# Kernel tuning notes

Hardware: AMD Instinct MI355X
Metric: run time of the kernel (lower is better)

Reference implementation:

```python
import jax, jax.numpy as jnp
import numpy as np

N, K, D = 32768, 8192, 256


def setup_inputs() -> dict:
    key = jax.random.key(0)
    k1, k2 = jax.random.split(key)
    x = jax.random.normal(k1, (N, D), dtype=jnp.float32)
    vectors = jax.random.normal(k2, (K, D), dtype=jnp.float32)  # codebook
    return {"x": x, "vectors": vectors}


def reference(x, vectors):
    # torch.cdist(x[:,None,:], vectors[None]) followed by argmin over K.
    # Euclidean distance is monotone in squared distance, so argmin over the
    # without a sqrt, matching the original math exactly for the returned ids.
    x2 = jnp.sum(x * x, axis=-1, keepdims=True)          # [N, 1]
    c2 = jnp.sum(vectors * vectors, axis=-1)             # [K]
    d2 = x2 + c2 - 2.0 * jnp.matmul(x, vectors.T)        # [N, K]
    indices = jnp.argmin(d2, axis=-1)                    # [N]
    return indices.astype(jnp.int32)
```

## Files before the change

kernel.cpp:

```cpp
#include <hip/hip_runtime.h>
#include <stdint.h>
#include <stddef.h>


#define N_PTS 32768
#define K_CB  8192
#define D_DIM 256
#define TM 128
#define TN 128
#define SPLITK 4
#define KCHUNK (K_CB / SPLITK)
#define NTILES (KCHUNK / TN)

#define WS_XH   0
#define WS_XL   (WS_XH + N_PTS * D_DIM * 2)
#define WS_CH   (WS_XL + N_PTS * D_DIM * 2)
#define WS_CL   (WS_CH + K_CB * D_DIM * 2)
#define WS_C2   (WS_CL + K_CB * D_DIM * 2)
#define WS_PD   (WS_C2 + K_CB * 4)
#define WS_PI   (WS_PD + SPLITK * N_PTS * 4)
#define WS_END  (WS_PI + SPLITK * N_PTS * 4)

typedef _Float16 half4v __attribute__((ext_vector_type(4)));
typedef _Float16 half8v __attribute__((ext_vector_type(8)));
typedef float    f32x4  __attribute__((ext_vector_type(4)));

__device__ __forceinline__ void gld16(const void* g, void* l) {
    __builtin_amdgcn_global_load_lds(
        (const __attribute__((address_space(1))) void*)g,
        (__attribute__((address_space(3))) void*)l, 16, 0, 0);
}


__global__ void __launch_bounds__(256)
split_kernel(const float* __restrict__ src, _Float16* __restrict__ h_out,
             _Float16* __restrict__ l_out) {
    const int i = blockIdx.x * 256 + threadIdx.x;
    const float4 v = ((const float4*)src)[i];
    half4v h = {(_Float16)v.x, (_Float16)v.y, (_Float16)v.z, (_Float16)v.w};
    half4v l = {(_Float16)((v.x - (float)h[0]) * 2048.0f),
                (_Float16)((v.y - (float)h[1]) * 2048.0f),
                (_Float16)((v.z - (float)h[2]) * 2048.0f),
                (_Float16)((v.w - (float)h[3]) * 2048.0f)};
    *(half4v*)(h_out + (size_t)i * 4) = h;
    *(half4v*)(l_out + (size_t)i * 4) = l;
}

__global__ void __launch_bounds__(256)
cnorms_kernel(const float* __restrict__ vecs, float* __restrict__ c2) {
    int gwave = (blockIdx.x * 256 + threadIdx.x) >> 6;
    int lane  = threadIdx.x & 63;
    const float* src = vecs + (size_t)gwave * D_DIM;
    float4 v = ((const float4*)src)[lane];
    float s = v.x * v.x + v.y * v.y + v.z * v.z + v.w * v.w;
#pragma unroll
    for (int off = 32; off > 0; off >>= 1) s += __shfl_down(s, off, 64);
    if (lane == 0) c2[gwave] = s;
}


__global__ void __launch_bounds__(256, 2)
vq_main_fast(const _Float16* __restrict__ xh_g, const _Float16* __restrict__ xl_g,
             const _Float16* __restrict__ ch_g, const _Float16* __restrict__ cl_g,
             const float* __restrict__ c2, float* __restrict__ pd, int* __restrict__ pi) {
    __shared__ __align__(16) char lds[65536];

    const int t    = threadIdx.x;
    const int lane = t & 63;
    const int wv   = t >> 6;
    const int wy   = wv >> 1, wx = wv & 1;
    const int fr   = lane & 15;
    const int g    = lane >> 4;

    const int split = blockIdx.x & (SPLITK - 1);
    const int pbase = (blockIdx.x >> 2) * TM;
    const int kbase = split * KCHUNK;

    const int rowoff = (lane >> 3) * (D_DIM * 2) + (((lane & 7) ^ (lane >> 3)) << 4);
    const char* xh_w = (const char*)xh_g + (size_t)(pbase + wv * 32) * (D_DIM * 2) + rowoff;
    const char* xl_w = (const char*)xl_g + (size_t)(pbase + wv * 32) * (D_DIM * 2) + rowoff;
    char* ldsA_h = lds +         (wv * 32) * 128;
    char* ldsA_l = lds + 16384 + (wv * 32) * 128;
    char* ldsB_h = lds + 32768 + (wv * 32) * 128;
    char* ldsB_l = lds + 49152 + (wv * 32) * 128;

    int aoff[4][2], boff[4][2];
#pragma unroll
    for (int i = 0; i < 4; ++i)
#pragma unroll
        for (int ks = 0; ks < 2; ++ks) {
            aoff[i][ks] = (wy * 64 + i * 16 + fr) * 128 + (((ks * 4 + g) ^ (fr & 7)) << 4);
            boff[i][ks] = 32768 + (wx * 64 + i * 16 + fr) * 128 + (((ks * 4 + g) ^ (fr & 7)) << 4);
        }

    float best[16];
    int   bidx[16];
#pragma unroll
    for (int i = 0; i < 16; ++i) { best[i] = 3.4e38f; bidx[i] = 0; }

    for (int kt = 0; kt < NTILES; ++kt) {
        const int ktbase = kbase + kt * TN;
        const char* ch_w = (const char*)ch_g + (size_t)(ktbase + wv * 32) * (D_DIM * 2) + rowoff;
        const char* cl_w = (const char*)cl_g + (size_t)(ktbase + wv * 32) * (D_DIM * 2) + rowoff;

        f32x4 acc[4][4];
#pragma unroll
        for (int i = 0; i < 4; ++i)
#pragma unroll
            for (int j = 0; j < 4; ++j) {
                f32x4 z = {0.f, 0.f, 0.f, 0.f};
                acc[i][j] = z;
            }

#pragma unroll 1
        for (int dkc = 0; dkc < 4; ++dkc) {
            const int gofs = dkc * 128;
            __syncthreads();
#pragma unroll
            for (int q = 0; q < 4; ++q) {
                gld16(xh_w + q * 4096 + gofs, ldsA_h + q * 1024);
                gld16(xl_w + q * 4096 + gofs, ldsA_l + q * 1024);
                gld16(ch_w + q * 4096 + gofs, ldsB_h + q * 1024);
                gld16(cl_w + q * 4096 + gofs, ldsB_l + q * 1024);
            }
            __syncthreads();
#pragma unroll
            for (int ks = 0; ks < 2; ++ks) {
                half8v a1[4], a2[4], a3[4];
#pragma unroll
                for (int i = 0; i < 4; ++i) {
                    const char* p = lds + aoff[i][ks];
                    a1[i] = *(const half8v*)p;
                    a3[i] = *(const half8v*)(p + 16384);
                    a2[i] = a1[i] * (_Float16)4.8828125e-4f;
                }
#pragma unroll
                for (int j = 0; j < 4; ++j) {
                    const char* p = lds + boff[j][ks];
                    half8v b1 = *(const half8v*)p;
                    half8v b2 = *(const half8v*)(p + 16384);
                    half8v b3 = b1 * (_Float16)4.8828125e-4f;
#pragma unroll
                    for (int i = 0; i < 4; ++i) {
                        acc[i][j] = __builtin_amdgcn_mfma_f32_16x16x32_f16(a1[i], b1, acc[i][j], 0, 0, 0);
                        acc[i][j] = __builtin_amdgcn_mfma_f32_16x16x32_f16(a2[i], b2, acc[i][j], 0, 0, 0);
                        acc[i][j] = __builtin_amdgcn_mfma_f32_16x16x32_f16(a3[i], b3, acc[i][j], 0, 0, 0);
                    }
                }
            }
        }

#pragma unroll
        for (int j = 0; j < 4; ++j) {
            const int cg = ktbase + wx * 64 + j * 16 + fr;
            const float c2v = c2[cg];
#pragma unroll
            for (int i = 0; i < 4; ++i)
#pragma unroll
                for (int r = 0; r < 4; ++r) {
                    const float v = fmaf(-2.0f, acc[i][j][r], c2v);
                    const int s = i * 4 + r;
                    if (v < best[s]) { best[s] = v; bidx[s] = cg; }
                }
        }
    }

    __syncthreads();
    float* rd = (float*)lds;
    int*   ri = (int*)lds + 256;
#pragma unroll
    for (int i = 0; i < 4; ++i)
#pragma unroll
        for (int r = 0; r < 4; ++r) {
            float bv = best[i * 4 + r];
            int   bi = bidx[i * 4 + r];
#pragma unroll
            for (int off = 1; off < 16; off <<= 1) {
                const float ov = __shfl_xor(bv, off, 64);
                const int   oi = __shfl_xor(bi, off, 64);
                if (ov < bv || (ov == bv && oi < bi)) { bv = ov; bi = oi; }
            }
            if (fr == 0) {
                const int rowl = wy * 64 + i * 16 + g * 4 + r;
                rd[rowl * 2 + wx] = bv;
                ri[rowl * 2 + wx] = bi;
            }
        }
    __syncthreads();
    if (t < TM) {
        float b0 = rd[t * 2];
        int   i0 = ri[t * 2];
        const float b1 = rd[t * 2 + 1];
        const int   i1 = ri[t * 2 + 1];
        if (b1 < b0 || (b1 == b0 && i1 < i0)) { b0 = b1; i0 = i1; }
        pd[split * N_PTS + pbase + t] = b0;
        pi[split * N_PTS + pbase + t] = i0;
    }
}


#define BK 32
#define LS (BK + 4)

__device__ inline half8v load8(const _Float16* p) {
    half4v a = *(const half4v*)p;
    half4v b = *(const half4v*)(p + 4);
    return __builtin_shufflevector(a, b, 0, 1, 2, 3, 4, 5, 6, 7);
}

struct Trip { _Float16 h, s2, l2; };

__device__ inline Trip cvt3(float v) {
    Trip t;
    _Float16 hh = (_Float16)v;
    float hf = (float)hh;
    t.h  = hh;
    t.s2 = (_Float16)(hf * 4.8828125e-4f);
    t.l2 = (_Float16)((v - hf) * 2048.0f);
    return t;
}

__global__ void __launch_bounds__(256, 2)
vq_main_v3(const float* __restrict__ x, const float* __restrict__ vecs,
           const float* __restrict__ c2, float* __restrict__ pd, int* __restrict__ pi) {
    __shared__ _Float16 lds[6 * TM * LS];
    _Float16* xh  = lds;
    _Float16* xs2 = lds + 1 * TM * LS;
    _Float16* xl2 = lds + 2 * TM * LS;
    _Float16* ch  = lds + 3 * TM * LS;
    _Float16* cl2 = lds + 4 * TM * LS;
    _Float16* cs2 = lds + 5 * TM * LS;

    const int t     = threadIdx.x;
    const int split = blockIdx.x & (SPLITK - 1);
    const int pbase = (blockIdx.x >> 2) * TM;
    const int kbase = split * KCHUNK;

    const int lane = t & 63;
    const int wv   = t >> 6;
    const int wy   = wv >> 1, wx = wv & 1;
    const int fr   = lane & 15;
    const int g    = lane >> 4;
    const int kb   = g * 8;

    const int srow = t >> 3;
    const int sc4  = (t & 7) * 4;

    float best[16];
    int   bidx[16];
#pragma unroll
    for (int i = 0; i < 16; ++i) { best[i] = 3.4e38f; bidx[i] = 0; }

    for (int kt = 0; kt < NTILES; ++kt) {
        const int ktbase = kbase + kt * TN;
        f32x4 acc[4][4];
#pragma unroll
        for (int i = 0; i < 4; ++i)
#pragma unroll
            for (int j = 0; j < 4; ++j) {
                f32x4 z = {0.f, 0.f, 0.f, 0.f};
                acc[i][j] = z;
            }
        for (int dk = 0; dk < D_DIM; dk += BK) {
            __syncthreads();
#pragma unroll
            for (int p = 0; p < 4; ++p) {
                const int row = srow + p * 32;
                const float4 v = *(const float4*)&x[(size_t)(pbase + row) * D_DIM + dk + sc4];
                const Trip t0 = cvt3(v.x), t1 = cvt3(v.y), t2 = cvt3(v.z), t3 = cvt3(v.w);
                half4v h  = {t0.h,  t1.h,  t2.h,  t3.h};
                half4v s2 = {t0.s2, t1.s2, t2.s2, t3.s2};
                half4v l2 = {t0.l2, t1.l2, t2.l2, t3.l2};
                *(half4v*)&xh [row * LS + sc4] = h;
                *(half4v*)&xs2[row * LS + sc4] = s2;
                *(half4v*)&xl2[row * LS + sc4] = l2;
                const float4 w = *(const float4*)&vecs[(size_t)(ktbase + row) * D_DIM + dk + sc4];
                const Trip u0 = cvt3(w.x), u1 = cvt3(w.y), u2 = cvt3(w.z), u3 = cvt3(w.w);
                half4v hc = {u0.h,  u1.h,  u2.h,  u3.h};
                half4v sc = {u0.s2, u1.s2, u2.s2, u3.s2};
                half4v lc = {u0.l2, u1.l2, u2.l2, u3.l2};
                *(half4v*)&ch [row * LS + sc4] = hc;
                *(half4v*)&cs2[row * LS + sc4] = sc;
                *(half4v*)&cl2[row * LS + sc4] = lc;
            }
            __syncthreads();
            half8v a1[4], a2[4], a3[4], b1[4], b2[4], b3[4];
#pragma unroll
            for (int i = 0; i < 4; ++i) {
                const int aoff = (wy * 64 + i * 16 + fr) * LS + kb;
                a1[i] = load8(&xh [aoff]);
                a2[i] = load8(&xs2[aoff]);
                a3[i] = load8(&xl2[aoff]);
                const int boff2 = (wx * 64 + i * 16 + fr) * LS + kb;
                b1[i] = load8(&ch [boff2]);
                b2[i] = load8(&cl2[boff2]);
                b3[i] = load8(&cs2[boff2]);
            }
#pragma unroll
            for (int i = 0; i < 4; ++i)
#pragma unroll
                for (int j = 0; j < 4; ++j) {
                    acc[i][j] = __builtin_amdgcn_mfma_f32_16x16x32_f16(a1[i], b1[j], acc[i][j], 0, 0, 0);
                    acc[i][j] = __builtin_amdgcn_mfma_f32_16x16x32_f16(a2[i], b2[j], acc[i][j], 0, 0, 0);
                    acc[i][j] = __builtin_amdgcn_mfma_f32_16x16x32_f16(a3[i], b3[j], acc[i][j], 0, 0, 0);
                }
        }
#pragma unroll
        for (int j = 0; j < 4; ++j) {
            const int cg = ktbase + wx * 64 + j * 16 + fr;
            const float c2v = c2[cg];
#pragma unroll
            for (int i = 0; i < 4; ++i)
#pragma unroll
                for (int r = 0; r < 4; ++r) {
                    const float v = fmaf(-2.0f, acc[i][j][r], c2v);
                    const int s = i * 4 + r;
                    if (v < best[s]) { best[s] = v; bidx[s] = cg; }
                }
        }
    }
    __syncthreads();
    float* rd = (float*)lds;
    int*   ri = (int*)lds + 256;
#pragma unroll
    for (int i = 0; i < 4; ++i)
#pragma unroll
        for (int r = 0; r < 4; ++r) {
            float bv = best[i * 4 + r];
            int   bi = bidx[i * 4 + r];
#pragma unroll
            for (int off = 1; off < 16; off <<= 1) {
                const float ov = __shfl_xor(bv, off, 64);
                const int   oi = __shfl_xor(bi, off, 64);
                if (ov < bv || (ov == bv && oi < bi)) { bv = ov; bi = oi; }
            }
            if (fr == 0) {
                const int rowl = wy * 64 + i * 16 + g * 4 + r;
                rd[rowl * 2 + wx] = bv;
                ri[rowl * 2 + wx] = bi;
            }
        }
    __syncthreads();
    if (t < TM) {
        float b0 = rd[t * 2];
        int   i0 = ri[t * 2];
        const float b1 = rd[t * 2 + 1];
        const int   i1 = ri[t * 2 + 1];
        if (b1 < b0 || (b1 == b0 && i1 < i0)) { b0 = b1; i0 = i1; }
        pd[split * N_PTS + pbase + t] = b0;
        pi[split * N_PTS + pbase + t] = i0;
    }
}


__global__ void __launch_bounds__(256)
vq_combine(const float* __restrict__ pd, const int* __restrict__ pi,
           int* __restrict__ out) {
    const int p = blockIdx.x * 256 + threadIdx.x;
    float bb = pd[p];
    int   bi = pi[p];
#pragma unroll
    for (int s = 1; s < SPLITK; ++s) {
        const float v  = pd[s * N_PTS + p];
        const int   vi = pi[s * N_PTS + p];
        if (v < bb || (v == bb && vi < bi)) { bb = v; bi = vi; }
    }
    out[p] = bi;
}

extern "C" void kernel_launch(void* const* d_in, const int* in_sizes, int n_in,
                              void* d_out, int out_size, void* d_ws, size_t ws_size,
                              hipStream_t stream) {
    const float* x    = (const float*)d_in[0];
    const float* vecs = (const float*)d_in[1];
    int* out = (int*)d_out;
    char* ws = (char*)d_ws;

    if (ws_size >= (size_t)WS_END) {
        _Float16* xh = (_Float16*)(ws + WS_XH);
        _Float16* xl = (_Float16*)(ws + WS_XL);
        _Float16* ch = (_Float16*)(ws + WS_CH);
        _Float16* cl = (_Float16*)(ws + WS_CL);
        float* c2 = (float*)(ws + WS_C2);
        float* pd = (float*)(ws + WS_PD);
        int*   pi = (int*)(ws + WS_PI);

        hipLaunchKernelGGL(split_kernel, dim3(N_PTS * D_DIM / 4 / 256), dim3(256), 0, stream,
                           x, xh, xl);
        hipLaunchKernelGGL(split_kernel, dim3(K_CB * D_DIM / 4 / 256), dim3(256), 0, stream,
                           vecs, ch, cl);
        hipLaunchKernelGGL(cnorms_kernel, dim3(K_CB / 4), dim3(256), 0, stream,
                           vecs, c2);
        hipLaunchKernelGGL(vq_main_fast, dim3((N_PTS / TM) * SPLITK), dim3(256), 0, stream,
                           xh, xl, ch, cl, c2, pd, pi);
        hipLaunchKernelGGL(vq_combine, dim3(N_PTS / 256), dim3(256), 0, stream,
                           pd, pi, out);
    } else {
        float* c2 = (float*)ws;
        float* pd = (float*)ws + K_CB;
        int*   pi = (int*)((float*)ws + K_CB + SPLITK * N_PTS);
        hipLaunchKernelGGL(cnorms_kernel, dim3(K_CB / 4), dim3(256), 0, stream,
                           vecs, c2);
        hipLaunchKernelGGL(vq_main_v3, dim3((N_PTS / TM) * SPLITK), dim3(256), 0, stream,
                           x, vecs, c2, pd, pi);
        hipLaunchKernelGGL(vq_combine, dim3(N_PTS / 256), dim3(256), 0, stream,
                           pd, pi, out);
    }
}
```

Measured before the change: 464.4 us.

## Halve LDS tile depth for higher occupancy and fuse codebook split with norms

```diff
diff --git a/kernel.cpp b/kernel.cpp
--- a/kernel.cpp
+++ b/kernel.cpp
@@ -47,23 +47,30 @@
 }
 
 __global__ void __launch_bounds__(256)
-cnorms_kernel(const float* __restrict__ vecs, float* __restrict__ c2) {
-    int gwave = (blockIdx.x * 256 + threadIdx.x) >> 6;
-    int lane  = threadIdx.x & 63;
-    const float* src = vecs + (size_t)gwave * D_DIM;
-    float4 v = ((const float4*)src)[lane];
+csplit_norm(const float* __restrict__ vecs, _Float16* __restrict__ h_out,
+            _Float16* __restrict__ l_out, float* __restrict__ c2) {
+    const int row  = (blockIdx.x * 256 + threadIdx.x) >> 6;
+    const int lane = threadIdx.x & 63;
+    const float4 v = ((const float4*)(vecs + (size_t)row * D_DIM))[lane];
+    half4v h = {(_Float16)v.x, (_Float16)v.y, (_Float16)v.z, (_Float16)v.w};
+    half4v l = {(_Float16)((v.x - (float)h[0]) * 2048.0f),
+                (_Float16)((v.y - (float)h[1]) * 2048.0f),
+                (_Float16)((v.z - (float)h[2]) * 2048.0f),
+                (_Float16)((v.w - (float)h[3]) * 2048.0f)};
+    *(half4v*)(h_out + (size_t)row * D_DIM + lane * 4) = h;
+    *(half4v*)(l_out + (size_t)row * D_DIM + lane * 4) = l;
     float s = v.x * v.x + v.y * v.y + v.z * v.z + v.w * v.w;
 #pragma unroll
     for (int off = 32; off > 0; off >>= 1) s += __shfl_down(s, off, 64);
-    if (lane == 0) c2[gwave] = s;
-}
-
-
-__global__ void __launch_bounds__(256, 2)
+    if (lane == 0) c2[row] = s;
+}
+
+
+__global__ void __launch_bounds__(256, 4)
 vq_main_fast(const _Float16* __restrict__ xh_g, const _Float16* __restrict__ xl_g,
              const _Float16* __restrict__ ch_g, const _Float16* __restrict__ cl_g,
              const float* __restrict__ c2, float* __restrict__ pd, int* __restrict__ pi) {
-    __shared__ __align__(16) char lds[65536];
+    __shared__ __align__(16) char lds[32768];
 
     const int t    = threadIdx.x;
     const int lane = t & 63;
@@ -76,22 +83,20 @@
     const int pbase = (blockIdx.x >> 2) * TM;
     const int kbase = split * KCHUNK;
 
-    const int rowoff = (lane >> 3) * (D_DIM * 2) + (((lane & 7) ^ (lane >> 3)) << 4);
+    const int rowoff = (lane >> 2) * (D_DIM * 2) + (((lane & 3) ^ ((lane >> 2) & 3)) << 4);
     const char* xh_w = (const char*)xh_g + (size_t)(pbase + wv * 32) * (D_DIM * 2) + rowoff;
     const char* xl_w = (const char*)xl_g + (size_t)(pbase + wv * 32) * (D_DIM * 2) + rowoff;
-    char* ldsA_h = lds +         (wv * 32) * 128;
-    char* ldsA_l = lds + 16384 + (wv * 32) * 128;
-    char* ldsB_h = lds + 32768 + (wv * 32) * 128;
-    char* ldsB_l = lds + 49152 + (wv * 32) * 128;
-
-    int aoff[4][2], boff[4][2];
-#pragma unroll
-    for (int i = 0; i < 4; ++i)
-#pragma unroll
-        for (int ks = 0; ks < 2; ++ks) {
-            aoff[i][ks] = (wy * 64 + i * 16 + fr) * 128 + (((ks * 4 + g) ^ (fr & 7)) << 4);
-            boff[i][ks] = 32768 + (wx * 64 + i * 16 + fr) * 128 + (((ks * 4 + g) ^ (fr & 7)) << 4);
-        }
+    char* ldsA_h = lds +         wv * 2048;
+    char* ldsA_l = lds +  8192 + wv * 2048;
+    char* ldsB_h = lds + 16384 + wv * 2048;
+    char* ldsB_l = lds + 24576 + wv * 2048;
+
+    int aoff[4], boff[4];
+#pragma unroll
+    for (int i = 0; i < 4; ++i) {
+        aoff[i] = (wy * 64 + i * 16 + fr) * 64 + ((g ^ (fr & 3)) << 4);
+        boff[i] = 16384 + (wx * 64 + i * 16 + fr) * 64 + ((g ^ (fr & 3)) << 4);
+    }
 
     float best[16];
     int   bidx[16];
@@ -113,39 +118,36 @@
             }
 
 #pragma unroll 1
-        for (int dkc = 0; dkc < 4; ++dkc) {
-            const int gofs = dkc * 128;
+        for (int dkc = 0; dkc < 8; ++dkc) {
+            const int gofs = dkc * 64;
             __syncthreads();
 #pragma unroll
-            for (int q = 0; q < 4; ++q) {
-                gld16(xh_w + q * 4096 + gofs, ldsA_h + q * 1024);
-                gld16(xl_w + q * 4096 + gofs, ldsA_l + q * 1024);
-                gld16(ch_w + q * 4096 + gofs, ldsB_h + q * 1024);
-                gld16(cl_w + q * 4096 + gofs, ldsB_l + q * 1024);
+            for (int q = 0; q < 2; ++q) {
+                gld16(xh_w + q * 8192 + gofs, ldsA_h + q * 1024);
+                gld16(xl_w + q * 8192 + gofs, ldsA_l + q * 1024);
+                gld16(ch_w + q * 8192 + gofs, ldsB_h + q * 1024);
+                gld16(cl_w + q * 8192 + gofs, ldsB_l + q * 1024);
             }
             __syncthreads();
-#pragma unroll
-            for (int ks = 0; ks < 2; ++ks) {
-                half8v a1[4], a2[4], a3[4];
+            half8v a1[4], a2[4], a3[4];
+#pragma unroll
+            for (int i = 0; i < 4; ++i) {
+                const char* p = lds + aoff[i];
+                a1[i] = *(const half8v*)p;
+                a3[i] = *(const half8v*)(p + 8192);
+                a2[i] = a1[i] * (_Float16)4.8828125e-4f;
+            }
+#pragma unroll
+            for (int j = 0; j < 4; ++j) {
+                const char* p = lds + boff[j];
+                half8v b1 = *(const half8v*)p;
+                half8v b2 = *(const half8v*)(p + 8192);
+                half8v b3 = b1 * (_Float16)4.8828125e-4f;
 #pragma unroll
                 for (int i = 0; i < 4; ++i) {
-                    const char* p = lds + aoff[i][ks];
-                    a1[i] = *(const half8v*)p;
-                    a3[i] = *(const half8v*)(p + 16384);
-                    a2[i] = a1[i] * (_Float16)4.8828125e-4f;
-                }
-#pragma unroll
-                for (int j = 0; j < 4; ++j) {
-                    const char* p = lds + boff[j][ks];
-                    half8v b1 = *(const half8v*)p;
-                    half8v b2 = *(const half8v*)(p + 16384);
-                    half8v b3 = b1 * (_Float16)4.8828125e-4f;
-#pragma unroll
-                    for (int i = 0; i < 4; ++i) {
-                        acc[i][j] = __builtin_amdgcn_mfma_f32_16x16x32_f16(a1[i], b1, acc[i][j], 0, 0, 0);
-                        acc[i][j] = __builtin_amdgcn_mfma_f32_16x16x32_f16(a2[i], b2, acc[i][j], 0, 0, 0);
-                        acc[i][j] = __builtin_amdgcn_mfma_f32_16x16x32_f16(a3[i], b3, acc[i][j], 0, 0, 0);
-                    }
+                    acc[i][j] = __builtin_amdgcn_mfma_f32_16x16x32_f16(a1[i], b1, acc[i][j], 0, 0, 0);
+                    acc[i][j] = __builtin_amdgcn_mfma_f32_16x16x32_f16(a2[i], b2, acc[i][j], 0, 0, 0);
+                    acc[i][j] = __builtin_amdgcn_mfma_f32_16x16x32_f16(a3[i], b3, acc[i][j], 0, 0, 0);
                 }
             }
         }
@@ -199,8 +201,8 @@
 }
 
 
-#define BK 32
-#define LS (BK + 4)
+#define FBK 32
+#define FLS (FBK + 4)
 
 __device__ inline half8v load8(const _Float16* p) {
     half4v a = *(const half4v*)p;
@@ -223,13 +225,13 @@
 __global__ void __launch_bounds__(256, 2)
 vq_main_v3(const float* __restrict__ x, const float* __restrict__ vecs,
            const float* __restrict__ c2, float* __restrict__ pd, int* __restrict__ pi) {
-    __shared__ _Float16 lds[6 * TM * LS];
+    __shared__ _Float16 lds[6 * TM * FLS];
     _Float16* xh  = lds;
-    _Float16* xs2 = lds + 1 * TM * LS;
-    _Float16* xl2 = lds + 2 * TM * LS;
-    _Float16* ch  = lds + 3 * TM * LS;
-    _Float16* cl2 = lds + 4 * TM * LS;
-    _Float16* cs2 = lds + 5 * TM * LS;
+    _Float16* xs2 = lds + 1 * TM * FLS;
+    _Float16* xl2 = lds + 2 * TM * FLS;
+    _Float16* ch  = lds + 3 * TM * FLS;
+    _Float16* cl2 = lds + 4 * TM * FLS;
+    _Float16* cs2 = lds + 5 * TM * FLS;
 
     const int t     = threadIdx.x;
     const int split = blockIdx.x & (SPLITK - 1);
@@ -261,7 +263,7 @@
                 f32x4 z = {0.f, 0.f, 0.f, 0.f};
                 acc[i][j] = z;
             }
-        for (int dk = 0; dk < D_DIM; dk += BK) {
+        for (int dk = 0; dk < D_DIM; dk += FBK) {
             __syncthreads();
 #pragma unroll
             for (int p = 0; p < 4; ++p) {
@@ -271,27 +273,27 @@
                 half4v h  = {t0.h,  t1.h,  t2.h,  t3.h};
                 half4v s2 = {t0.s2, t1.s2, t2.s2, t3.s2};
                 half4v l2 = {t0.l2, t1.l2, t2.l2, t3.l2};
-                *(half4v*)&xh [row * LS + sc4] = h;
-                *(half4v*)&xs2[row * LS + sc4] = s2;
-                *(half4v*)&xl2[row * LS + sc4] = l2;
+                *(half4v*)&xh [row * FLS + sc4] = h;
+                *(half4v*)&xs2[row * FLS + sc4] = s2;
+                *(half4v*)&xl2[row * FLS + sc4] = l2;
                 const float4 w = *(const float4*)&vecs[(size_t)(ktbase + row) * D_DIM + dk + sc4];
                 const Trip u0 = cvt3(w.x), u1 = cvt3(w.y), u2 = cvt3(w.z), u3 = cvt3(w.w);
                 half4v hc = {u0.h,  u1.h,  u2.h,  u3.h};
                 half4v sc = {u0.s2, u1.s2, u2.s2, u3.s2};
                 half4v lc = {u0.l2, u1.l2, u2.l2, u3.l2};
-                *(half4v*)&ch [row * LS + sc4] = hc;
-                *(half4v*)&cs2[row * LS + sc4] = sc;
-                *(half4v*)&cl2[row * LS + sc4] = lc;
+                *(half4v*)&ch [row * FLS + sc4] = hc;
+                *(half4v*)&cs2[row * FLS + sc4] = sc;
+                *(half4v*)&cl2[row * FLS + sc4] = lc;
             }
             __syncthreads();
             half8v a1[4], a2[4], a3[4], b1[4], b2[4], b3[4];
 #pragma unroll
             for (int i = 0; i < 4; ++i) {
-                const int aoff = (wy * 64 + i * 16 + fr) * LS + kb;
+                const int aoff = (wy * 64 + i * 16 + fr) * FLS + kb;
                 a1[i] = load8(&xh [aoff]);
                 a2[i] = load8(&xs2[aoff]);
                 a3[i] = load8(&xl2[aoff]);
-                const int boff2 = (wx * 64 + i * 16 + fr) * LS + kb;
+                const int boff2 = (wx * 64 + i * 16 + fr) * FLS + kb;
                 b1[i] = load8(&ch [boff2]);
                 b2[i] = load8(&cl2[boff2]);
                 b3[i] = load8(&cs2[boff2]);
@@ -387,10 +389,8 @@
 
         hipLaunchKernelGGL(split_kernel, dim3(N_PTS * D_DIM / 4 / 256), dim3(256), 0, stream,
                            x, xh, xl);
-        hipLaunchKernelGGL(split_kernel, dim3(K_CB * D_DIM / 4 / 256), dim3(256), 0, stream,
-                           vecs, ch, cl);
-        hipLaunchKernelGGL(cnorms_kernel, dim3(K_CB / 4), dim3(256), 0, stream,
-                           vecs, c2);
+        hipLaunchKernelGGL(csplit_norm, dim3(K_CB / 4), dim3(256), 0, stream,
+                           vecs, ch, cl, c2);
         hipLaunchKernelGGL(vq_main_fast, dim3((N_PTS / TM) * SPLITK), dim3(256), 0, stream,
                            xh, xl, ch, cl, c2, pd, pi);
         hipLaunchKernelGGL(vq_combine, dim3(N_PTS / 256), dim3(256), 0, stream,
@@ -399,8 +399,9 @@
         float* c2 = (float*)ws;
         float* pd = (float*)ws + K_CB;
         int*   pi = (int*)((float*)ws + K_CB + SPLITK * N_PTS);
-        hipLaunchKernelGGL(cnorms_kernel, dim3(K_CB / 4), dim3(256), 0, stream,
-                           vecs, c2);
+        hipLaunchKernelGGL(csplit_norm, dim3(K_CB / 4), dim3(256), 0, stream,
+                           vecs, (_Float16*)((float*)ws + K_CB + 2 * SPLITK * N_PTS),
+                           (_Float16*)((float*)ws + K_CB + 2 * SPLITK * N_PTS) + K_CB * D_DIM, c2);
         hipLaunchKernelGGL(vq_main_v3, dim3((N_PTS / TM) * SPLITK), dim3(256), 0, stream,
                            x, vecs, c2, pd, pi);
         hipLaunchKernelGGL(vq_combine, dim3(N_PTS / 256), dim3(256), 0, stream,
```

After: 620.0 us. +33.5%, slower.
